# Optimization experiments

Hardware: AMD Instinct MI355X
Metric: run time of the kernel (lower is better)

The kernel has to match this reference:

```python
import jax, jax.numpy as jnp
import numpy as np

D = 128        # node_representation_size
V = 100000     # unique_internal_nodes (embedding vocab)
N = 20000      # nodes in the internal graph
E = 640000     # total neighbor (edge) entries


def setup_inputs() -> dict:
    key = jax.random.key(0)
    k1, k2, k3, k4, k5, k6 = jax.random.split(key, 6)
    node_ids = jax.random.randint(k1, (N,), 0, V)
    neighbor_ids = jax.random.randint(k2, (E,), 0, V)
    segment_ids = jnp.sort(jax.random.randint(k3, (E,), 0, N))
    xav = 1.0 / np.sqrt(D)  # xavier_normal std for square [D,D]
    W = jax.random.normal(k4, (D, D), dtype=jnp.float32) * xav
    M = jax.random.normal(k5, (D, D), dtype=jnp.float32) * xav
    emb = jax.random.normal(k6, (V, D), dtype=jnp.float32)
    return {"node_ids": node_ids, "neighbor_ids": neighbor_ids,
            "segment_ids": segment_ids, "W": W, "M": M, "emb": emb}


def reference(node_ids, neighbor_ids, segment_ids, W, M, emb):
    # Per node: s = relu(W @ e[node] + sum_{nbr} M @ e[nbr]); result = sum_nodes s
    self_term = emb[node_ids] @ W.T                       # [N, D]
    nb_msgs = emb[neighbor_ids] @ M.T                     # [E, D]
    nb_agg = jax.ops.segment_sum(nb_msgs, segment_ids, num_segments=N)  # [N, D]
    per_node = jax.nn.relu(self_term + nb_agg)            # [N, D]
    result = per_node.sum(axis=0)                         # [D]
    return jax.nn.softmax(result)[:, None]                # [D, 1], softmax over dim 0
```

## Files before the change

kernel.cpp:

```cpp
#include <hip/hip_runtime.h>

#define D 128
#define RS_STRIDE 64

typedef __attribute__((ext_vector_type(8))) short bf16x8;
typedef __attribute__((ext_vector_type(8))) unsigned short u16x8;
typedef __attribute__((ext_vector_type(4))) float f32x4;

__device__ __forceinline__ unsigned short f2bf(float f) {
    unsigned u = __float_as_uint(f);
    unsigned r = (u + 0x7fffu + ((u >> 16) & 1u)) >> 16;
    return (unsigned short)r;
}
__device__ __forceinline__ float bf2f(unsigned short h) {
    return __uint_as_float(((unsigned)h) << 16);
}
__device__ __forceinline__ ushort4 pack4(float4 v) {
    ushort4 o; o.x = f2bf(v.x); o.y = f2bf(v.y); o.z = f2bf(v.z); o.w = f2bf(v.w);
    return o;
}
__device__ __forceinline__ void red3(float& x) {
    x += __shfl_xor(x, 8);
    x += __shfl_xor(x, 16);
    x += __shfl_xor(x, 32);
}

__global__ void convert_kernel(const float* __restrict__ emb, const float* __restrict__ W,
                               const float* __restrict__ M, unsigned short* __restrict__ embb,
                               unsigned short* __restrict__ Wb, unsigned short* __restrict__ Mb,
                               float* __restrict__ rs, int n4) {
    int i = blockIdx.x * blockDim.x + threadIdx.x;
    if (i < n4) ((ushort4*)embb)[i] = pack4(((const float4*)emb)[i]);
    if (i < 4096)       ((ushort4*)Wb)[i]        = pack4(((const float4*)W)[i]);
    else if (i < 8192)  ((ushort4*)Mb)[i - 4096] = pack4(((const float4*)M)[i - 4096]);
    if (i < D) rs[i * RS_STRIDE] = 0.0f;
}

__global__ void rowptr_kernel(const int* __restrict__ seg, int* __restrict__ row_ptr,
                              int E, int N) {
    int e = blockIdx.x * blockDim.x + threadIdx.x;
    if (e >= E) return;
    int s = seg[e];
    if (e == 0) {
        for (int n = 0; n <= s; ++n) row_ptr[n] = 0;
    } else {
        int sp = seg[e - 1];
        for (int n = sp + 1; n <= s; ++n) row_ptr[n] = e;
    }
    if (e == E - 1) {
        for (int n = s + 1; n <= N; ++n) row_ptr[n] = E;
    }
}

__global__ void agg_bf_kernel(const int* __restrict__ nbr, const int* __restrict__ row_ptr,
                              const unsigned short* __restrict__ embb,
                              unsigned short* __restrict__ aggb, int N) {
    int n = blockIdx.x * 4 + (threadIdx.x >> 6);
    if (n >= N) return;
    int tt = threadIdx.x & 63;
    int c = tt & 7;
    int j = tt >> 3;

    int lo = row_ptr[n], hi = row_ptr[n + 1];

    float s0[8], s1[8];
#pragma unroll
    for (int k = 0; k < 8; ++k) { s0[k] = 0.f; s1[k] = 0.f; }

    for (int e = lo + j; e < hi; e += 8) {
        const u16x8* r = (const u16x8*)(embb + (size_t)nbr[e] * D);
        u16x8 v0 = r[c];
        u16x8 v1 = r[c + 8];
#pragma unroll
        for (int k = 0; k < 8; ++k) { s0[k] += bf2f(v0[k]); s1[k] += bf2f(v1[k]); }
    }
#pragma unroll
    for (int k = 0; k < 8; ++k) { red3(s0[k]); red3(s1[k]); }

    if (j == 0) {
        u16x8 o0, o1;
#pragma unroll
        for (int k = 0; k < 8; ++k) { o0[k] = f2bf(s0[k]); o1[k] = f2bf(s1[k]); }
        u16x8* o = (u16x8*)(aggb + (size_t)n * D);
        o[c] = o0;
        o[c + 8] = o1;
    }
}

__global__ void agg_f32_kernel(const int* __restrict__ nbr, const int* __restrict__ row_ptr,
                               const float* __restrict__ emb,
                               unsigned short* __restrict__ aggb, int N) {
    int n = blockIdx.x * 4 + (threadIdx.x >> 6);
    if (n >= N) return;
    int tt = threadIdx.x & 63;
    int c = tt & 7;
    int j = tt >> 3;

    int lo = row_ptr[n], hi = row_ptr[n + 1];

    float4 s0 = make_float4(0.f, 0.f, 0.f, 0.f);
    float4 s1 = make_float4(0.f, 0.f, 0.f, 0.f);
    float4 s2 = make_float4(0.f, 0.f, 0.f, 0.f);
    float4 s3 = make_float4(0.f, 0.f, 0.f, 0.f);
    for (int e = lo + j; e < hi; e += 8) {
        const float4* r = (const float4*)&emb[(size_t)nbr[e] * D];
        float4 v0 = r[c], v1 = r[c + 8], v2 = r[c + 16], v3 = r[c + 24];
        s0.x += v0.x; s0.y += v0.y; s0.z += v0.z; s0.w += v0.w;
        s1.x += v1.x; s1.y += v1.y; s1.z += v1.z; s1.w += v1.w;
        s2.x += v2.x; s2.y += v2.y; s2.z += v2.z; s2.w += v2.w;
        s3.x += v3.x; s3.y += v3.y; s3.z += v3.z; s3.w += v3.w;
    }
    red3(s0.x); red3(s0.y); red3(s0.z); red3(s0.w);
    red3(s1.x); red3(s1.y); red3(s1.z); red3(s1.w);
    red3(s2.x); red3(s2.y); red3(s2.z); red3(s2.w);
    red3(s3.x); red3(s3.y); red3(s3.z); red3(s3.w);
    if (j == 0) {
        ushort4* o = (ushort4*)(aggb + (size_t)n * D);
        o[c]      = pack4(s0);
        o[c + 8]  = pack4(s1);
        o[c + 16] = pack4(s2);
        o[c + 24] = pack4(s3);
    }
}

template <bool BF>
__global__ __launch_bounds__(256) void matvec_kernel(
    const int* __restrict__ node_ids, const void* __restrict__ embv,
    const unsigned short* __restrict__ aggb,
    const unsigned short* __restrict__ Wb, const unsigned short* __restrict__ Mb,
    float* __restrict__ rs, int N, int ngroups, int nstripes) {
    int t = threadIdx.x;
    int wid = blockIdx.x * 4 + (t >> 6);
    int l = t & 63;
    int quad = l >> 4, col = l & 15;
    int dt = wid & 7;
    int stripe = wid >> 3;

    bf16x8 bw[4], bm[4];
    int wrow = (dt * 16 + col) * D;
#pragma unroll
    for (int ks = 0; ks < 4; ++ks) {
        int off = wrow + ks * 32 + quad * 8;
        bw[ks] = *(const bf16x8*)(Wb + off);
        bm[ks] = *(const bf16x8*)(Mb + off);
    }

    const bf16x8 zero8 = {0, 0, 0, 0, 0, 0, 0, 0};
    float vsum = 0.f;

    for (int grp = stripe; grp < ngroups; grp += nstripes) {
        int node = grp * 16 + col;
        bool valid = node < N;
        int nid = valid ? node_ids[node] : 0;
        const unsigned short* ar = aggb + (size_t)node * D + quad * 8;

        f32x4 acc = {0.f, 0.f, 0.f, 0.f};
#pragma unroll
        for (int ks = 0; ks < 4; ++ks) {
            bf16x8 ax;
            if (BF) {
                const unsigned short* xr =
                    (const unsigned short*)embv + (size_t)nid * D + quad * 8;
                ax = valid ? *(const bf16x8*)(xr + ks * 32) : zero8;
            } else {
                if (valid) {
                    const float4* xf = (const float4*)((const float*)embv +
                                       (size_t)nid * D + quad * 8 + ks * 32);
                    ushort4 p0 = pack4(xf[0]);
                    ushort4 p1 = pack4(xf[1]);
                    ax[0] = (short)p0.x; ax[1] = (short)p0.y;
                    ax[2] = (short)p0.z; ax[3] = (short)p0.w;
                    ax[4] = (short)p1.x; ax[5] = (short)p1.y;
                    ax[6] = (short)p1.z; ax[7] = (short)p1.w;
                } else ax = zero8;
            }
            bf16x8 aa = valid ? *(const bf16x8*)(ar + ks * 32) : zero8;
            acc = __builtin_amdgcn_mfma_f32_16x16x32_bf16(ax, bw[ks], acc, 0, 0, 0);
            acc = __builtin_amdgcn_mfma_f32_16x16x32_bf16(aa, bm[ks], acc, 0, 0, 0);
        }
        vsum += fmaxf(acc[0], 0.f) + fmaxf(acc[1], 0.f)
              + fmaxf(acc[2], 0.f) + fmaxf(acc[3], 0.f);
    }

    vsum += __shfl_xor(vsum, 16);
    vsum += __shfl_xor(vsum, 32);
    if (l < 16) atomicAdd(&rs[(dt * 16 + col) * RS_STRIDE], vsum);
}

__global__ void softmax_kernel(const float* __restrict__ rs, float* __restrict__ out) {
    int t = threadIdx.x;
    float v0 = rs[t * RS_STRIDE];
    float v1 = rs[(t + 64) * RS_STRIDE];
    float m = fmaxf(v0, v1);
    for (int o = 32; o > 0; o >>= 1) m = fmaxf(m, __shfl_xor(m, o));
    float e0 = expf(v0 - m);
    float e1 = expf(v1 - m);
    float s = e0 + e1;
    for (int o = 32; o > 0; o >>= 1) s += __shfl_xor(s, o);
    float inv = 1.0f / s;
    out[t] = e0 * inv;
    out[t + 64] = e1 * inv;
}

extern "C" void kernel_launch(void* const* d_in, const int* in_sizes, int n_in,
                              void* d_out, int out_size, void* d_ws, size_t ws_size,
                              hipStream_t stream) {
    const int*   node_ids = (const int*)d_in[0];
    const int*   nbr      = (const int*)d_in[1];
    const int*   seg      = (const int*)d_in[2];
    const float* W        = (const float*)d_in[3];
    const float* M        = (const float*)d_in[4];
    const float* emb      = (const float*)d_in[5];
    float* out = (float*)d_out;

    int N = in_sizes[0];
    int E = in_sizes[1];
    long long VD = in_sizes[5];
    int ngroups  = (N + 15) / 16;
    int nstripes = (ngroups + 1) / 2;
    int mv_blocks = 2 * nstripes;

    unsigned short* aggb = (unsigned short*)d_ws;
    unsigned short* Wb   = aggb + (size_t)N * D;
    unsigned short* Mb   = Wb + D * D;
    float* rs            = (float*)(Mb + D * D);
    int* row_ptr         = (int*)(rs + (size_t)D * RS_STRIDE);
    unsigned short* embb = (unsigned short*)(row_ptr + (N + 1));

    size_t need_bf = (size_t)(row_ptr + (N + 1) - (int*)d_ws) * 4 + (size_t)VD * 2;
    bool use_bf = ws_size >= need_bf;
    int n4 = use_bf ? (int)(VD / 4) : 0;
    int cvt_n = (n4 > 8192 ? n4 : 8192);

    convert_kernel<<<(cvt_n + 255) / 256, 256, 0, stream>>>(emb, W, M, embb, Wb, Mb, rs, n4);
    rowptr_kernel<<<(E + 255) / 256, 256, 0, stream>>>(seg, row_ptr, E, N);
    if (use_bf) {
        agg_bf_kernel<<<(N + 3) / 4, 256, 0, stream>>>(nbr, row_ptr, embb, aggb, N);
        matvec_kernel<true><<<mv_blocks, 256, 0, stream>>>(node_ids, embb, aggb, Wb, Mb,
                                                           rs, N, ngroups, nstripes);
    } else {
        agg_f32_kernel<<<(N + 3) / 4, 256, 0, stream>>>(nbr, row_ptr, emb, aggb, N);
        matvec_kernel<false><<<mv_blocks, 256, 0, stream>>>(node_ids, emb, aggb, Wb, Mb,
                                                            rs, N, ngroups, nstripes);
    }
    softmax_kernel<<<1, 64, 0, stream>>>(rs, out);
}
```

Baseline: 155.2 us.

## Fuse neighbor aggregation with MFMA matvec and merge prep kernels

Merges the convert and row_ptr kernels into a single prep launch. Replaces the separate aggregation and matvec kernels with one fused kernel per 16-node group. That kernel gathers self and neighbor embeddings into swizzled LDS tiles, then runs bf16 MFMA against W and M with ReLU and an atomic row-sum. This removes the global round trip of the aggregated bf16 buffer and two launches. The neighbor loop is also unrolled by two to keep more loads in flight, at the cost of less parallelism per node during gathering and more atomics to rs.

```diff
diff --git a/kernel.cpp b/kernel.cpp
--- a/kernel.cpp
+++ b/kernel.cpp
@@ -24,66 +24,128 @@
     x += __shfl_xor(x, 16);
     x += __shfl_xor(x, 32);
 }
-
-__global__ void convert_kernel(const float* __restrict__ emb, const float* __restrict__ W,
-                               const float* __restrict__ M, unsigned short* __restrict__ embb,
-                               unsigned short* __restrict__ Wb, unsigned short* __restrict__ Mb,
-                               float* __restrict__ rs, int n4) {
+__device__ __forceinline__ int swz(int r, int s) {
+    return r * D + ((s ^ (r & 7)) << 3);
+}
+
+__global__ void prep_kernel(const float* __restrict__ emb, const float* __restrict__ W,
+                            const float* __restrict__ M, const int* __restrict__ seg,
+                            unsigned short* __restrict__ embb,
+                            unsigned short* __restrict__ Wb, unsigned short* __restrict__ Mb,
+                            float* __restrict__ rs, int* __restrict__ row_ptr,
+                            int n4, int E, int N) {
     int i = blockIdx.x * blockDim.x + threadIdx.x;
     if (i < n4) ((ushort4*)embb)[i] = pack4(((const float4*)emb)[i]);
     if (i < 4096)       ((ushort4*)Wb)[i]        = pack4(((const float4*)W)[i]);
     else if (i < 8192)  ((ushort4*)Mb)[i - 4096] = pack4(((const float4*)M)[i - 4096]);
     if (i < D) rs[i * RS_STRIDE] = 0.0f;
-}
-
-__global__ void rowptr_kernel(const int* __restrict__ seg, int* __restrict__ row_ptr,
-                              int E, int N) {
-    int e = blockIdx.x * blockDim.x + threadIdx.x;
-    if (e >= E) return;
-    int s = seg[e];
-    if (e == 0) {
-        for (int n = 0; n <= s; ++n) row_ptr[n] = 0;
-    } else {
-        int sp = seg[e - 1];
-        for (int n = sp + 1; n <= s; ++n) row_ptr[n] = e;
-    }
-    if (e == E - 1) {
-        for (int n = s + 1; n <= N; ++n) row_ptr[n] = E;
-    }
-}
-
-__global__ void agg_bf_kernel(const int* __restrict__ nbr, const int* __restrict__ row_ptr,
-                              const unsigned short* __restrict__ embb,
-                              unsigned short* __restrict__ aggb, int N) {
-    int n = blockIdx.x * 4 + (threadIdx.x >> 6);
-    if (n >= N) return;
-    int tt = threadIdx.x & 63;
-    int c = tt & 7;
-    int j = tt >> 3;
-
-    int lo = row_ptr[n], hi = row_ptr[n + 1];
-
-    float s0[8], s1[8];
-#pragma unroll
-    for (int k = 0; k < 8; ++k) { s0[k] = 0.f; s1[k] = 0.f; }
-
-    for (int e = lo + j; e < hi; e += 8) {
-        const u16x8* r = (const u16x8*)(embb + (size_t)nbr[e] * D);
-        u16x8 v0 = r[c];
-        u16x8 v1 = r[c + 8];
-#pragma unroll
-        for (int k = 0; k < 8; ++k) { s0[k] += bf2f(v0[k]); s1[k] += bf2f(v1[k]); }
-    }
-#pragma unroll
-    for (int k = 0; k < 8; ++k) { red3(s0[k]); red3(s1[k]); }
-
-    if (j == 0) {
-        u16x8 o0, o1;
-#pragma unroll
-        for (int k = 0; k < 8; ++k) { o0[k] = f2bf(s0[k]); o1[k] = f2bf(s1[k]); }
-        u16x8* o = (u16x8*)(aggb + (size_t)n * D);
-        o[c] = o0;
-        o[c + 8] = o1;
+    if (i < E) {
+        int s = seg[i];
+        if (i == 0) {
+            for (int n = 0; n <= s; ++n) row_ptr[n] = 0;
+        } else {
+            int sp = seg[i - 1];
+            for (int n = sp + 1; n <= s; ++n) row_ptr[n] = i;
+        }
+        if (i == E - 1) {
+            for (int n = s + 1; n <= N; ++n) row_ptr[n] = E;
+        }
+    }
+}
+
+__global__ __launch_bounds__(256) void fused_kernel(
+    const int* __restrict__ node_ids, const int* __restrict__ nbr,
+    const int* __restrict__ row_ptr, const unsigned short* __restrict__ embb,
+    const unsigned short* __restrict__ Wb, const unsigned short* __restrict__ Mb,
+    float* __restrict__ rs, int N) {
+    __shared__ unsigned short xs[16 * D];
+    __shared__ unsigned short as_[16 * D];
+
+    int t = threadIdx.x;
+    int w = t >> 6;
+    int tt = t & 63;
+    int g = blockIdx.x;
+
+    {
+        int c = tt & 7;
+        int j = tt >> 3;
+        for (int i = 0; i < 4; ++i) {
+            int r = w * 4 + i;
+            int n = g * 16 + r;
+            bool valid = n < N;
+
+            if (j == 0) {
+                u16x8 x0 = {0, 0, 0, 0, 0, 0, 0, 0}, x1 = x0;
+                if (valid) {
+                    const u16x8* xr = (const u16x8*)(embb + (size_t)node_ids[n] * D);
+                    x0 = xr[c]; x1 = xr[c + 8];
+                }
+                *(u16x8*)&xs[swz(r, c)]     = x0;
+                *(u16x8*)&xs[swz(r, c + 8)] = x1;
+            }
+
+            float s0[8], s1[8];
+#pragma unroll
+            for (int k = 0; k < 8; ++k) { s0[k] = 0.f; s1[k] = 0.f; }
+
+            int lo = valid ? row_ptr[n] : 0;
+            int hi = valid ? row_ptr[n + 1] : 0;
+            int e = lo + j;
+            for (; e + 8 < hi; e += 16) {
+                const u16x8* ra = (const u16x8*)(embb + (size_t)nbr[e] * D);
+                const u16x8* rb = (const u16x8*)(embb + (size_t)nbr[e + 8] * D);
+                u16x8 a0 = ra[c], a1 = ra[c + 8];
+                u16x8 b0 = rb[c], b1 = rb[c + 8];
+#pragma unroll
+                for (int k = 0; k < 8; ++k) {
+                    s0[k] += bf2f(a0[k]) + bf2f(b0[k]);
+                    s1[k] += bf2f(a1[k]) + bf2f(b1[k]);
+                }
+            }
+            if (e < hi) {
+                const u16x8* ra = (const u16x8*)(embb + (size_t)nbr[e] * D);
+                u16x8 a0 = ra[c], a1 = ra[c + 8];
+#pragma unroll
+                for (int k = 0; k < 8; ++k) { s0[k] += bf2f(a0[k]); s1[k] += bf2f(a1[k]); }
+            }
+#pragma unroll
+            for (int k = 0; k < 8; ++k) { red3(s0[k]); red3(s1[k]); }
+
+            if (j == 0) {
+                u16x8 o0, o1;
+#pragma unroll
+                for (int k = 0; k < 8; ++k) { o0[k] = f2bf(s0[k]); o1[k] = f2bf(s1[k]); }
+                *(u16x8*)&as_[swz(r, c)]     = o0;
+                *(u16x8*)&as_[swz(r, c + 8)] = o1;
+            }
+        }
+    }
+    __syncthreads();
+
+    int quad = tt >> 4, col = tt & 15;
+    bf16x8 ax[4], aa[4];
+#pragma unroll
+    for (int ks = 0; ks < 4; ++ks) {
+        ax[ks] = *(const bf16x8*)&xs[swz(col, ks * 4 + quad)];
+        aa[ks] = *(const bf16x8*)&as_[swz(col, ks * 4 + quad)];
+    }
+#pragma unroll
+    for (int p = 0; p < 2; ++p) {
+        int dt = w + p * 4;
+        int wrow = (dt * 16 + col) * D + quad * 8;
+        f32x4 acc = {0.f, 0.f, 0.f, 0.f};
+#pragma unroll
+        for (int ks = 0; ks < 4; ++ks) {
+            bf16x8 bw = *(const bf16x8*)(Wb + wrow + ks * 32);
+            bf16x8 bm = *(const bf16x8*)(Mb + wrow + ks * 32);
+            acc = __builtin_amdgcn_mfma_f32_16x16x32_bf16(ax[ks], bw, acc, 0, 0, 0);
+            acc = __builtin_amdgcn_mfma_f32_16x16x32_bf16(aa[ks], bm, acc, 0, 0, 0);
+        }
+        float v = fmaxf(acc[0], 0.f) + fmaxf(acc[1], 0.f)
+                + fmaxf(acc[2], 0.f) + fmaxf(acc[3], 0.f);
+        v += __shfl_xor(v, 16);
+        v += __shfl_xor(v, 32);
+        if (tt < 16) atomicAdd(&rs[(dt * 16 + col) * RS_STRIDE], v);
     }
 }
 
@@ -217,8 +279,6 @@
     int E = in_sizes[1];
     long long VD = in_sizes[5];
     int ngroups  = (N + 15) / 16;
-    int nstripes = (ngroups + 1) / 2;
-    int mv_blocks = 2 * nstripes;
 
     unsigned short* aggb = (unsigned short*)d_ws;
     unsigned short* Wb   = aggb + (size_t)N * D;
@@ -231,17 +291,18 @@
     bool use_bf = ws_size >= need_bf;
     int n4 = use_bf ? (int)(VD / 4) : 0;
     int cvt_n = (n4 > 8192 ? n4 : 8192);
-
-    convert_kernel<<<(cvt_n + 255) / 256, 256, 0, stream>>>(emb, W, M, embb, Wb, Mb, rs, n4);
-    rowptr_kernel<<<(E + 255) / 256, 256, 0, stream>>>(seg, row_ptr, E, N);
+    int prep_n = (cvt_n > E ? cvt_n : E);
+
+    prep_kernel<<<(prep_n + 255) / 256, 256, 0, stream>>>(emb, W, M, seg, embb, Wb, Mb,
+                                                          rs, row_ptr, n4, E, N);
     if (use_bf) {
-        agg_bf_kernel<<<(N + 3) / 4, 256, 0, stream>>>(nbr, row_ptr, embb, aggb, N);
-        matvec_kernel<true><<<mv_blocks, 256, 0, stream>>>(node_ids, embb, aggb, Wb, Mb,
-                                                           rs, N, ngroups, nstripes);
+        fused_kernel<<<ngroups, 256, 0, stream>>>(node_ids, nbr, row_ptr, embb,
+                                                  Wb, Mb, rs, N);
     } else {
+        int nstripes = (ngroups + 1) / 2;
         agg_f32_kernel<<<(N + 3) / 4, 256, 0, stream>>>(nbr, row_ptr, emb, aggb, N);
-        matvec_kernel<false><<<mv_blocks, 256, 0, stream>>>(node_ids, emb, aggb, Wb, Mb,
-                                                            rs, N, ngroups, nstripes);
+        matvec_kernel<false><<<2 * nstripes, 256, 0, stream>>>(node_ids, emb, aggb, Wb, Mb,
+                                                               rs, N, ngroups, nstripes);
     }
     softmax_kernel<<<1, 64, 0, stream>>>(rs, out);
 }
```

New measurement: 152.7 us. About the same (-1.6%).
